# Performance work log

Hardware: AMD Instinct MI355X
Metric: run time of the kernel (lower is better)

Reference implementation:

```python
import math
import jax, jax.numpy as jnp
import numpy as np

S = 30.0          # cfg.MODEL.HEADS.SCALE
M = 0.5           # cfg.MODEL.HEADS.MARGIN
MOM = 0.5         # EMA momentum (hardcoded in module)
COS_M = math.cos(M)
SIN_M = math.sin(M)
THRESHOLD = math.cos(math.pi - M)
MM = math.sin(math.pi - M) * M
EPS = 1e-12       # F.normalize eps


def setup_inputs() -> dict:
    key = jax.random.key(0)
    k1, k2, k3 = jax.random.split(key, 3)
    B, D, C = 512, 256, 100000
    features = jax.random.normal(k1, (B, D), jnp.float32)
    targets = jax.random.randint(k2, (B,), 0, C, dtype=jnp.int32).astype(jnp.int64)
    weight = jax.random.normal(k3, (C, D), jnp.float32)
    weight = weight / jnp.maximum(jnp.linalg.norm(weight, axis=1, keepdims=True), EPS)
    t = jnp.zeros((1,), jnp.float32)
    return {"features": features, "targets": targets, "weight": weight, "t": t}


def reference(features, targets, weight, t):
    B = features.shape[0]
    C = weight.shape[0]
    rows = jnp.arange(B)

    # F.normalize(features, dim=1)
    f = features / jnp.maximum(jnp.linalg.norm(features, axis=1, keepdims=True), EPS)

    # cos_theta = f @ W.T   [B, C]
    cos_theta = jnp.einsum('bd,cd->bc', f, weight)

    # ArcFace margin on the target logit
    target_logit = cos_theta[rows, targets][:, None]              # [B, 1]
    sin_theta = jnp.sqrt(jnp.maximum(1.0 - target_logit ** 2, 0.0))
    cos_theta_m = target_logit * COS_M - sin_theta * SIN_M        # cos(theta + m)
    mask = cos_theta > cos_theta_m                                 # hard examples
    final_target_logit = jnp.where(target_logit > THRESHOLD,
                                   cos_theta_m, target_logit - MM)

    # EMA of mean target logit (buffer t), used immediately after update
    t_new = jnp.mean(target_logit) * 0.01 + 0.99 * t              # [1]

    # hard-example reweighting: cos[mask] = hard * (t + hard)
    cos_theta = jnp.where(mask, cos_theta * (t_new[0] + cos_theta), cos_theta)
    # scatter final target logit into the target column
    cos_theta = cos_theta.at[rows, targets].set(final_target_logit[:, 0])

    pred_class_logits = cos_theta * S

    # memory-bank EMA update: per-unique-target mean, EMA, renormalize (no_grad)
    fd = jax.lax.stop_gradient(f)
    counts = jax.ops.segment_sum(jnp.ones((B,), fd.dtype), targets, num_segments=C)
    sums = jax.ops.segment_sum(fd, targets, num_segments=C)        # [C, D]
    mean_w = sums / jnp.maximum(counts, 1.0)[:, None]
    upd = MOM * weight + (1.0 - MOM) * mean_w
    upd = upd / jnp.maximum(jnp.linalg.norm(upd, axis=1, keepdims=True), EPS)
    new_weight = jnp.where((counts > 0)[:, None], upd, weight)

    return pred_class_logits, new_weight, t_new
```

## Files before the change

kernel.cpp:

```cpp
#include <hip/hip_runtime.h>
#include <math.h>

#define B_SZ 512
#define D_SZ 256
#define C_SZ 100000
#define S_SCALE 30.0f
#define COS_Mc 0.8775825618903728f
#define SIN_Mc 0.479425538604203f
#define THRESHOLDc (-0.8775825618903728f)
#define MMc 0.2397127693021015f
#define EPSc 1e-12f

#define OUT_W_OFF ((size_t)B_SZ * C_SZ)
#define OUT_T_OFF (OUT_W_OFF + (size_t)C_SZ * D_SZ)

#define WSB_F 0
#define WSB_FHI 524288
#define WSB_FLO 786432
#define WSB_TL 1048576
#define WSB_CTM 1050624
#define WSB_FLT 1052672
#define WSB_TNEW 1054720

typedef __attribute__((ext_vector_type(8))) short bf16x8;
typedef __attribute__((ext_vector_type(4))) float f32x4;
typedef __attribute__((address_space(3))) void lds_void;
typedef const __attribute__((address_space(1))) void g_void;

__device__ __forceinline__ float wave_reduce_sum(float v) {
#pragma unroll
    for (int off = 32; off > 0; off >>= 1) v += __shfl_down(v, off, 64);
    return v;
}

__device__ __forceinline__ unsigned short f2bf(float x) {
    union { float f; unsigned u; } v; v.f = x;
    unsigned r = v.u + 0x7fff + ((v.u >> 16) & 1);
    return (unsigned short)(r >> 16);
}
__device__ __forceinline__ float bf2f(unsigned short h) {
    union { float f; unsigned u; } v;
    v.u = ((unsigned)h) << 16;
    return v.f;
}

__global__ __launch_bounds__(256) void prep_kernel(
    const float* __restrict__ features, const int* __restrict__ targets,
    const float* __restrict__ weight, float* __restrict__ f,
    unsigned short* __restrict__ fhi, unsigned short* __restrict__ flo,
    float* __restrict__ tl, float* __restrict__ ctm, float* __restrict__ flt) {
    int b = blockIdx.x;
    int d = threadIdx.x;
    float x = features[b * D_SZ + d];
    float v = wave_reduce_sum(x * x);
    __shared__ float red[4];
    int wave = d >> 6, lane = d & 63;
    if (lane == 0) red[wave] = v;
    __syncthreads();
    float s = red[0] + red[1] + red[2] + red[3];
    float scale = 1.0f / fmaxf(sqrtf(s), EPSc);
    float fv = x * scale;
    f[b * D_SZ + d] = fv;
    unsigned short h = f2bf(fv);
    fhi[b * D_SZ + d] = h;
    flo[b * D_SZ + d] = f2bf(fv - bf2f(h));

    int tgt = targets[b];
    float wv = weight[(size_t)tgt * D_SZ + d];
    float p = wave_reduce_sum(fv * wv);
    __syncthreads();
    if (lane == 0) red[wave] = p;
    __syncthreads();
    if (d == 0) {
        float t_l = red[0] + red[1] + red[2] + red[3];
        tl[b] = t_l;
        float sin_t = sqrtf(fmaxf(1.0f - t_l * t_l, 0.0f));
        float c_m = t_l * COS_Mc - sin_t * SIN_Mc;
        ctm[b] = c_m;
        flt[b] = (t_l > THRESHOLDc) ? c_m : (t_l - MMc);
    }
}

__global__ __launch_bounds__(512) void tnew_kernel(
    const float* __restrict__ tl, const float* __restrict__ t_in,
    float* __restrict__ tnew_ws, float* __restrict__ out_t) {
    int i = threadIdx.x;
    float v = wave_reduce_sum(tl[i]);
    __shared__ float red[8];
    int wave = i >> 6, lane = i & 63;
    if (lane == 0) red[wave] = v;
    __syncthreads();
    if (i == 0) {
        float s = 0.f;
#pragma unroll
        for (int w = 0; w < 8; w++) s += red[w];
        float tn = (s / (float)B_SZ) * 0.01f + 0.99f * t_in[0];
        tnew_ws[0] = tn;
        out_t[0] = tn;
    }
}

__global__ __launch_bounds__(256) void wpack_kernel(
    const float* __restrict__ w, unsigned short* __restrict__ whi,
    unsigned short* __restrict__ wlo) {
    size_t i = ((size_t)blockIdx.x * 256 + threadIdx.x) * 8;
    float4 a = *(const float4*)&w[i];
    float4 b = *(const float4*)&w[i + 4];
    union { unsigned short us[8]; bf16x8 v; } h, l;
    float xs[8] = {a.x, a.y, a.z, a.w, b.x, b.y, b.z, b.w};
#pragma unroll
    for (int j = 0; j < 8; j++) {
        unsigned short hh = f2bf(xs[j]);
        h.us[j] = hh;
        l.us[j] = f2bf(xs[j] - bf2f(hh));
    }
    *(bf16x8*)&whi[i] = h.v;
    *(bf16x8*)&wlo[i] = l.v;
}

__global__ __launch_bounds__(256) void gemm_kernel(
    const unsigned short* __restrict__ fhi, const unsigned short* __restrict__ flo,
    const unsigned short* __restrict__ whi, const unsigned short* __restrict__ wlo,
    const int* __restrict__ targets, const float* __restrict__ ctm,
    const float* __restrict__ flt, const float* __restrict__ tnew,
    float* __restrict__ out) {
    __shared__ unsigned short lds[4][128][32];

    const int t = threadIdx.x;
    const int w = t >> 6, l = t & 63;
    const int wr = w >> 1, wc = w & 1;
    const int fr = l & 15, kgrp = l >> 4;
    const int col0 = blockIdx.x * 128;
    const int row0 = blockIdx.y * 128;

    const unsigned short* gsrc[8];
    unsigned short* ldst[8];
    {
        int rsec = l >> 2;
        int slot = (l & 3) ^ ((l >> 3) & 3);
#pragma unroll
        for (int i = 0; i < 8; i++) {
            int ss = w + 4 * i;
            int buf = ss >> 3;
            int r0 = (ss & 7) * 16;
            int r = r0 + rsec;
            const unsigned short* base;
            int grow;
            if (buf == 0) { base = fhi; grow = row0 + r; }
            else if (buf == 1) { base = flo; grow = row0 + r; }
            else {
                int c = col0 + r;
                if (c > C_SZ - 1) c = C_SZ - 1;
                base = (buf == 2) ? whi : wlo;
                grow = c;
            }
            gsrc[i] = base + (size_t)grow * D_SZ + slot * 8;
            ldst[i] = &lds[buf][r0][0];
        }
    }

    const unsigned swz = ((unsigned)((fr >> 1) & 3)) << 4;
    const unsigned kb = ((unsigned)(kgrp * 16)) ^ swz;
    const char* aph = (const char*)&lds[0][0][0] + (unsigned)(wr * 64 + fr) * 64 + kb;
    const char* apl = (const char*)&lds[1][0][0] + (unsigned)(wr * 64 + fr) * 64 + kb;
    const char* bph = (const char*)&lds[2][0][0] + (unsigned)(wc * 64 + fr) * 64 + kb;
    const char* bpl = (const char*)&lds[3][0][0] + (unsigned)(wc * 64 + fr) * 64 + kb;

    f32x4 acc[4][4] = {};

    for (int kt = 0; kt < D_SZ; kt += 32) {
#pragma unroll
        for (int i = 0; i < 8; i++) {
            __builtin_amdgcn_global_load_lds((g_void*)(gsrc[i] + kt),
                                             (lds_void*)ldst[i], 16, 0, 0);
        }
        __syncthreads();

        bf16x8 ah[4], al[4];
#pragma unroll
        for (int mi = 0; mi < 4; mi++) {
            ah[mi] = *(const bf16x8*)(aph + mi * 1024);
            al[mi] = *(const bf16x8*)(apl + mi * 1024);
        }
#pragma unroll
        for (int ni = 0; ni < 4; ni++) {
            bf16x8 bh = *(const bf16x8*)(bph + ni * 1024);
            bf16x8 bl = *(const bf16x8*)(bpl + ni * 1024);
#pragma unroll
            for (int mi = 0; mi < 4; mi++) {
                acc[mi][ni] = __builtin_amdgcn_mfma_f32_16x16x32_bf16(
                    ah[mi], bh, acc[mi][ni], 0, 0, 0);
                acc[mi][ni] = __builtin_amdgcn_mfma_f32_16x16x32_bf16(
                    ah[mi], bl, acc[mi][ni], 0, 0, 0);
                acc[mi][ni] = __builtin_amdgcn_mfma_f32_16x16x32_bf16(
                    al[mi], bh, acc[mi][ni], 0, 0, 0);
            }
        }
        __syncthreads();
    }

    float tn = tnew[0];
#pragma unroll
    for (int mi = 0; mi < 4; mi++) {
#pragma unroll
        for (int j = 0; j < 4; j++) {
            int r = row0 + wr * 64 + mi * 16 + (l >> 4) * 4 + j;
            int tg = targets[r];
            float cm = ctm[r], fl = flt[r];
            size_t base = (size_t)r * C_SZ;
#pragma unroll
            for (int ni = 0; ni < 4; ni++) {
                int cg = col0 + wc * 64 + ni * 16;
                if (cg < C_SZ) {
                    int c = cg + fr;
                    float v = acc[mi][ni][j];
                    if (c == tg) v = fl;
                    else if (v > cm) v = v * (tn + v);
                    out[base + c] = v * S_SCALE;
                }
            }
        }
    }
}

__global__ __launch_bounds__(256) void copyw_kernel(
    const float4* __restrict__ src, float4* __restrict__ dst, int n4) {
    int i = blockIdx.x * blockDim.x + threadIdx.x;
    if (i < n4) dst[i] = src[i];
}

__global__ __launch_bounds__(256) void updw_kernel(
    const int* __restrict__ targets, const float* __restrict__ f,
    const float* __restrict__ weight, float* __restrict__ outw) {
    __shared__ int tg[B_SZ];
    __shared__ int dup;
    int t = threadIdx.x;
    if (t == 0) dup = 0;
    tg[t] = targets[t];
    tg[t + 256] = targets[t + 256];
    __syncthreads();
    int b = blockIdx.x;
    int c = tg[b];
    if ((t < b && tg[t] == c) || (t + 256 < b && tg[t + 256] == c)) dup = 1;
    __syncthreads();
    if (dup) return;

    float sum = 0.f;
    int cnt = 0;
    for (int i = b; i < B_SZ; i++) {
        if (tg[i] == c) { sum += f[i * D_SZ + t]; cnt++; }
    }
    float mean = sum / (float)cnt;
    float upd = 0.5f * weight[(size_t)c * D_SZ + t] + 0.5f * mean;
    float v = wave_reduce_sum(upd * upd);
    __shared__ float red[4];
    int wave = t >> 6, lane = t & 63;
    if (lane == 0) red[wave] = v;
    __syncthreads();
    float s = red[0] + red[1] + red[2] + red[3];
    float nrm = fmaxf(sqrtf(s), EPSc);
    outw[(size_t)c * D_SZ + t] = upd / nrm;
}

extern "C" void kernel_launch(void* const* d_in, const int* in_sizes, int n_in,
                              void* d_out, int out_size, void* d_ws, size_t ws_size,
                              hipStream_t stream) {
    const float* features = (const float*)d_in[0];
    const int* targets = (const int*)d_in[1];
    const float* weight = (const float*)d_in[2];
    const float* t_in = (const float*)d_in[3];
    float* out = (float*)d_out;
    char* wsb = (char*)d_ws;

    float* f = (float*)(wsb + WSB_F);
    unsigned short* fhi = (unsigned short*)(wsb + WSB_FHI);
    unsigned short* flo = (unsigned short*)(wsb + WSB_FLO);
    float* tl = (float*)(wsb + WSB_TL);
    float* ctm = (float*)(wsb + WSB_CTM);
    float* flt = (float*)(wsb + WSB_FLT);
    float* tnew = (float*)(wsb + WSB_TNEW);

    unsigned short* whi = (unsigned short*)(out + OUT_W_OFF);
    unsigned short* wlo = whi + (size_t)C_SZ * D_SZ;

    prep_kernel<<<B_SZ, 256, 0, stream>>>(features, targets, weight, f, fhi, flo,
                                          tl, ctm, flt);
    tnew_kernel<<<1, 512, 0, stream>>>(tl, t_in, tnew, out + OUT_T_OFF);

    wpack_kernel<<<12500, 256, 0, stream>>>(weight, whi, wlo);

    dim3 ggrid((C_SZ + 127) / 128, B_SZ / 128);
    gemm_kernel<<<ggrid, 256, 0, stream>>>(fhi, flo, whi, wlo, targets, ctm, flt,
                                           tnew, out);

    int n4 = (C_SZ * D_SZ) / 4;
    copyw_kernel<<<(n4 + 255) / 256, 256, 0, stream>>>(
        (const float4*)weight, (float4*)(out + OUT_W_OFF), n4);

    updw_kernel<<<B_SZ, 256, 0, stream>>>(targets, f, weight, out + OUT_W_OFF);
}
```

Before: 582.2 us.

## Fuse weight bf16 hi/lo split into GEMM B-tile loading

Drops the separate wpack kernel that converted the fp32 weight into bf16 hi/lo arrays in global memory. The GEMM now reads fp32 weight directly, splits it into hi/lo in registers and writes both halves into LDS. It also prefetches the next k-slice of weight into registers while the MFMAs run. This removes a full extra read and write pass over the 100 MB weight, but reads fp32 weight (twice the bytes of bf16) in each of the four row-block tiles and adds conversion ALU work inside the GEMM.

```diff
diff --git a/kernel.cpp b/kernel.cpp
--- a/kernel.cpp
+++ b/kernel.cpp
@@ -100,27 +100,9 @@
     }
 }
 
-__global__ __launch_bounds__(256) void wpack_kernel(
-    const float* __restrict__ w, unsigned short* __restrict__ whi,
-    unsigned short* __restrict__ wlo) {
-    size_t i = ((size_t)blockIdx.x * 256 + threadIdx.x) * 8;
-    float4 a = *(const float4*)&w[i];
-    float4 b = *(const float4*)&w[i + 4];
-    union { unsigned short us[8]; bf16x8 v; } h, l;
-    float xs[8] = {a.x, a.y, a.z, a.w, b.x, b.y, b.z, b.w};
-#pragma unroll
-    for (int j = 0; j < 8; j++) {
-        unsigned short hh = f2bf(xs[j]);
-        h.us[j] = hh;
-        l.us[j] = f2bf(xs[j] - bf2f(hh));
-    }
-    *(bf16x8*)&whi[i] = h.v;
-    *(bf16x8*)&wlo[i] = l.v;
-}
-
 __global__ __launch_bounds__(256) void gemm_kernel(
     const unsigned short* __restrict__ fhi, const unsigned short* __restrict__ flo,
-    const unsigned short* __restrict__ whi, const unsigned short* __restrict__ wlo,
+    const float* __restrict__ weight,
     const int* __restrict__ targets, const float* __restrict__ ctm,
     const float* __restrict__ flt, const float* __restrict__ tnew,
     float* __restrict__ out) {
@@ -133,31 +115,32 @@
     const int col0 = blockIdx.x * 128;
     const int row0 = blockIdx.y * 128;
 
-    const unsigned short* gsrc[8];
-    unsigned short* ldst[8];
+    const unsigned short* gsrcA[4];
+    unsigned short* ldstA[4];
     {
         int rsec = l >> 2;
         int slot = (l & 3) ^ ((l >> 3) & 3);
 #pragma unroll
-        for (int i = 0; i < 8; i++) {
+        for (int i = 0; i < 4; i++) {
             int ss = w + 4 * i;
             int buf = ss >> 3;
             int r0 = (ss & 7) * 16;
-            int r = r0 + rsec;
-            const unsigned short* base;
-            int grow;
-            if (buf == 0) { base = fhi; grow = row0 + r; }
-            else if (buf == 1) { base = flo; grow = row0 + r; }
-            else {
-                int c = col0 + r;
-                if (c > C_SZ - 1) c = C_SZ - 1;
-                base = (buf == 2) ? whi : wlo;
-                grow = c;
-            }
-            gsrc[i] = base + (size_t)grow * D_SZ + slot * 8;
-            ldst[i] = &lds[buf][r0][0];
-        }
-    }
+            const unsigned short* base = buf ? flo : fhi;
+            gsrcA[i] = base + (size_t)(row0 + r0 + rsec) * D_SZ + slot * 8;
+            ldstA[i] = &lds[buf][r0][0];
+        }
+    }
+
+    const int wrow_l = t >> 1;
+    const int wh = t & 1;
+    int wrow_g = col0 + wrow_l;
+    if (wrow_g > C_SZ - 1) wrow_g = C_SZ - 1;
+    const float* wbase = weight + (size_t)wrow_g * D_SZ + wh * 16;
+    const unsigned swzr = (((unsigned)wrow_l >> 1) & 3) << 4;
+    const unsigned bo0 = ((unsigned)wh * 32) ^ swzr;
+    const unsigned bo1 = ((unsigned)wh * 32 + 16) ^ swzr;
+    char* bhi_w = (char*)&lds[2][0][0] + (unsigned)wrow_l * 64;
+    char* blo_w = (char*)&lds[3][0][0] + (unsigned)wrow_l * 64;
 
     const unsigned swz = ((unsigned)((fr >> 1) & 3)) << 4;
     const unsigned kb = ((unsigned)(kgrp * 16)) ^ swz;
@@ -168,13 +151,41 @@
 
     f32x4 acc[4][4] = {};
 
+    float4 wv0 = *(const float4*)(wbase + 0);
+    float4 wv1 = *(const float4*)(wbase + 4);
+    float4 wv2 = *(const float4*)(wbase + 8);
+    float4 wv3 = *(const float4*)(wbase + 12);
+
     for (int kt = 0; kt < D_SZ; kt += 32) {
-#pragma unroll
-        for (int i = 0; i < 8; i++) {
-            __builtin_amdgcn_global_load_lds((g_void*)(gsrc[i] + kt),
-                                             (lds_void*)ldst[i], 16, 0, 0);
-        }
+        union { unsigned short us[8]; bf16x8 v; } h0, h1, l0, l1;
+        {
+            float xs[16] = {wv0.x, wv0.y, wv0.z, wv0.w, wv1.x, wv1.y, wv1.z, wv1.w,
+                            wv2.x, wv2.y, wv2.z, wv2.w, wv3.x, wv3.y, wv3.z, wv3.w};
+#pragma unroll
+            for (int j = 0; j < 8; j++) {
+                unsigned short hh = f2bf(xs[j]);
+                h0.us[j] = hh; l0.us[j] = f2bf(xs[j] - bf2f(hh));
+                unsigned short hh2 = f2bf(xs[j + 8]);
+                h1.us[j] = hh2; l1.us[j] = f2bf(xs[j + 8] - bf2f(hh2));
+            }
+        }
+        if (kt) __syncthreads();
+#pragma unroll
+        for (int i = 0; i < 4; i++)
+            __builtin_amdgcn_global_load_lds((g_void*)(gsrcA[i] + kt),
+                                             (lds_void*)ldstA[i], 16, 0, 0);
+        *(bf16x8*)(bhi_w + bo0) = h0.v;
+        *(bf16x8*)(bhi_w + bo1) = h1.v;
+        *(bf16x8*)(blo_w + bo0) = l0.v;
+        *(bf16x8*)(blo_w + bo1) = l1.v;
         __syncthreads();
+
+        if (kt + 32 < D_SZ) {
+            wv0 = *(const float4*)(wbase + kt + 32);
+            wv1 = *(const float4*)(wbase + kt + 36);
+            wv2 = *(const float4*)(wbase + kt + 40);
+            wv3 = *(const float4*)(wbase + kt + 44);
+        }
 
         bf16x8 ah[4], al[4];
 #pragma unroll
@@ -196,7 +207,6 @@
                     al[mi], bh, acc[mi][ni], 0, 0, 0);
             }
         }
-        __syncthreads();
     }
 
     float tn = tnew[0];
@@ -280,17 +290,12 @@
     float* flt = (float*)(wsb + WSB_FLT);
     float* tnew = (float*)(wsb + WSB_TNEW);
 
-    unsigned short* whi = (unsigned short*)(out + OUT_W_OFF);
-    unsigned short* wlo = whi + (size_t)C_SZ * D_SZ;
-
     prep_kernel<<<B_SZ, 256, 0, stream>>>(features, targets, weight, f, fhi, flo,
                                           tl, ctm, flt);
     tnew_kernel<<<1, 512, 0, stream>>>(tl, t_in, tnew, out + OUT_T_OFF);
 
-    wpack_kernel<<<12500, 256, 0, stream>>>(weight, whi, wlo);
-
     dim3 ggrid((C_SZ + 127) / 128, B_SZ / 128);
-    gemm_kernel<<<ggrid, 256, 0, stream>>>(fhi, flo, whi, wlo, targets, ctm, flt,
+    gemm_kernel<<<ggrid, 256, 0, stream>>>(fhi, flo, weight, targets, ctm, flt,
                                            tnew, out);
 
     int n4 = (C_SZ * D_SZ) / 4;
```

Measured after the change: 515.4 us. -11.5%, faster.
